# Optimization experiments

Measured on AMD Instinct MI355X. Metric: run time of the kernel, lower is better.

## Reference

```python
import jax, jax.numpy as jnp
import numpy as np

B, T, NUM_SKILLS, CONCEPT_NUM, HIDDEN = 64, 200, 1024, 256, 1024


def setup_inputs() -> dict:
    key = jax.random.key(0)
    ks = jax.random.split(key, 12)
    s_in = 1.0 / np.sqrt(NUM_SKILLS)
    s_h = 1.0 / np.sqrt(HIDDEN)
    s_c = 1.0 / np.sqrt(CONCEPT_NUM)
    return {
        "q_hot": jax.random.normal(ks[0], (B, T, NUM_SKILLS), jnp.float32),
        "result": jax.random.randint(ks[1], (B, T), 0, 2, jnp.int32),
        "next_q_hot": jax.random.normal(ks[2], (B, T, NUM_SKILLS), jnp.float32),
        "concept_num": CONCEPT_NUM,
        # kc: Linear(num_skills -> concept_num)
        "W_kc": jax.random.uniform(ks[3], (CONCEPT_NUM, NUM_SKILLS), jnp.float32, -s_in, s_in),
        "b_kc": jax.random.uniform(ks[4], (CONCEPT_NUM,), jnp.float32, -s_in, s_in),
        # LSTM (input = 2*concept_num, hidden = HIDDEN), torch gate order i,f,g,o
        "W_ih": jax.random.uniform(ks[5], (4 * HIDDEN, 2 * CONCEPT_NUM), jnp.float32, -s_h, s_h),
        "W_hh": jax.random.uniform(ks[6], (4 * HIDDEN, HIDDEN), jnp.float32, -s_h, s_h),
        "b_ih": jax.random.uniform(ks[7], (4 * HIDDEN,), jnp.float32, -s_h, s_h),
        "b_hh": jax.random.uniform(ks[8], (4 * HIDDEN,), jnp.float32, -s_h, s_h),
        # state: Linear(hidden -> concept_num)
        "W_state": jax.random.uniform(ks[9], (CONCEPT_NUM, HIDDEN), jnp.float32, -s_h, s_h),
        "b_state": jax.random.uniform(ks[10], (CONCEPT_NUM,), jnp.float32, -s_h, s_h),
        # out: Linear(concept_num -> 1)
        "W_out": jax.random.uniform(ks[11], (1, CONCEPT_NUM), jnp.float32, -s_c, s_c),
        "b_out": jax.random.uniform(jax.random.fold_in(key, 99), (1,), jnp.float32, -s_c, s_c),
    }


def _lstm(x, W_ih, W_hh, b_ih, b_hh):
    # x: [B, T, In] batch_first; returns h_seq [B, T, H]
    H = W_hh.shape[1]
    xT = jnp.swapaxes(x, 0, 1)                      # [T, B, In]
    gx = jnp.einsum('tbi,gi->tbg', xT, W_ih) + b_ih + b_hh  # [T, B, 4H]
    h0 = jnp.zeros((x.shape[0], H), x.dtype)
    c0 = jnp.zeros((x.shape[0], H), x.dtype)

    def step(carry, g_t):
        h, c = carry
        g = g_t + h @ W_hh.T                        # [B, 4H]
        i, f, gg, o = jnp.split(g, 4, axis=-1)
        i, f, o = jax.nn.sigmoid(i), jax.nn.sigmoid(f), jax.nn.sigmoid(o)
        c = f * c + i * jnp.tanh(gg)
        h = o * jnp.tanh(c)
        return (h, c), h

    _, h_seq = jax.lax.scan(step, (h0, c0), gx)
    return jnp.swapaxes(h_seq, 0, 1)                # [B, T, H]


def reference(q_hot, result, next_q_hot, concept_num,
              W_kc, b_kc, W_ih, W_hh, b_ih, b_hh,
              W_state, b_state, W_out, b_out):
    kc_hot = q_hot @ W_kc.T + b_kc                  # [B, T, C]
    next_kc_hot = next_q_hot @ W_kc.T + b_kc        # [B, T, C]

    # Vectorized replacement of the python double loop:
    # result==1 -> [kc_hot, 0]; else -> [0, kc_hot]
    mask = (result == 1)[..., None].astype(kc_hot.dtype)  # [B, T, 1]
    kc_vec = jnp.concatenate([kc_hot * mask, kc_hot * (1.0 - mask)], axis=-1)  # [B,T,2C]

    h = _lstm(kc_vec, W_ih, W_hh, b_ih, b_hh)       # [B, T, H]
    stu_state = h @ W_state.T + b_state             # [B, T, C]
    knowledge_div = stu_state - next_kc_hot
    vector = knowledge_div * next_kc_hot
    res = vector @ W_out.T + b_out                  # [B, T, 1]
    return (res, stu_state)
```

## Files before the change

kernel.cpp:

```cpp
#include <hip/hip_runtime.h>
#include <math.h>


typedef unsigned short u16;
typedef unsigned long long u64;
typedef __bf16 bf16x8 __attribute__((ext_vector_type(8)));
typedef float floatx4 __attribute__((ext_vector_type(4)));

__device__ __forceinline__ float bf2f(u16 h) {
  unsigned int u = ((unsigned int)h) << 16;
  float f;
  __builtin_memcpy(&f, &u, 4);
  return f;
}
__device__ __forceinline__ u16 f2bf(float f) {
  unsigned int u;
  __builtin_memcpy(&u, &f, 4);
  u += 0x7FFFu + ((u >> 16) & 1u);
  return (u16)(u >> 16);
}
__device__ __forceinline__ float sigm(float x) { return 1.0f / (1.0f + __expf(-x)); }

__global__ void cvt_kernel(const float* __restrict__ in, u16* __restrict__ out) {
  const int i = blockIdx.x * 256 + threadIdx.x;
  const float4 v = ((const float4*)in)[i];
  ushort4 o;
  o.x = f2bf(v.x);
  o.y = f2bf(v.y);
  o.z = f2bf(v.z);
  o.w = f2bf(v.w);
  ((ushort4*)out)[i] = o;
}

template <class Epi>
__global__ __launch_bounds__(256, 2) void gemm_bt(const u16* __restrict__ A,
                                                  const u16* __restrict__ B,
                                                  int M, int N, int K, Epi epi) {
  __shared__ u16 As[128 * 32];
  __shared__ u16 Bs[128 * 32];
  const int tid = threadIdx.x;
  const int w = tid >> 6, lane = tid & 63;
  const int wm = w & 1, wn = w >> 1;
  const int bm = blockIdx.x * 128, bn = blockIdx.y * 128;
  const int lrow = lane & 15, lk8 = (lane >> 4) * 8;
  const int srow = lane >> 2;
  const int skc = (lane & 3) * 8;

  floatx4 acc[4][4] = {};

  for (int k0 = 0; k0 < K; k0 += 32) {
#pragma unroll
    for (int r = 0; r < 2; ++r) {
      const int seg = w * 2 + r;
      const int row = seg * 16 + srow;
      __builtin_amdgcn_global_load_lds(
          (const __attribute__((address_space(1))) unsigned int*)(A + (size_t)(bm + row) * K + k0 + skc),
          (__attribute__((address_space(3))) unsigned int*)(As + seg * 512), 16, 0, 0);
      __builtin_amdgcn_global_load_lds(
          (const __attribute__((address_space(1))) unsigned int*)(B + (size_t)(bn + row) * K + k0 + skc),
          (__attribute__((address_space(3))) unsigned int*)(Bs + seg * 512), 16, 0, 0);
    }
    __syncthreads();

    bf16x8 af[4], bfr[4];
#pragma unroll
    for (int i = 0; i < 4; ++i) {
      af[i] = *(const bf16x8*)(As + (wm * 64 + i * 16 + lrow) * 32 + lk8);
      bfr[i] = *(const bf16x8*)(Bs + (wn * 64 + i * 16 + lrow) * 32 + lk8);
    }
#pragma unroll
    for (int i = 0; i < 4; ++i)
#pragma unroll
      for (int j = 0; j < 4; ++j)
        acc[i][j] = __builtin_amdgcn_mfma_f32_16x16x32_bf16(af[i], bfr[j], acc[i][j], 0, 0, 0);
    __syncthreads();
  }

  const int rbase = bm + wm * 64 + (lane >> 4) * 4;
  const int cbase = bn + wn * 64 + lrow;
#pragma unroll
  for (int i = 0; i < 4; ++i)
#pragma unroll
    for (int j = 0; j < 4; ++j)
#pragma unroll
      for (int r = 0; r < 4; ++r)
        epi(rbase + i * 16 + r, cbase + j * 16, acc[i][j][r]);
}

struct EpiKcVec {
  const float* bkc;
  const int* result;
  u16* kcv;
  __device__ void operator()(int row, int col, float v) const {
    v += bkc[col];
    const int off = (result[row] == 1) ? 0 : 256;
    const size_t base = (size_t)row * 512;
    kcv[base + off + col] = f2bf(v);
    kcv[base + (256 - off) + col] = 0;
  }
};
struct EpiNk {
  const float* bkc;
  float* nk;
  __device__ void operator()(int row, int col, float v) const {
    nk[(size_t)row * 256 + col] = v + bkc[col];
  }
};
struct EpiGx {
  const float* bih;
  const float* bhh;
  u16* gx;
  __device__ void operator()(int row, int col, float v) const {
    v += bih[col] + bhh[col];
    const int b = row / 200, t = row - b * 200;
    gx[(size_t)(t * 64 + b) * 4096 + col] = f2bf(v);
  }
};
struct EpiStu {
  const float* bst;
  float* out;
  __device__ void operator()(int row, int col, float v) const {
    v += bst[col];
    const int b = row & 63, t = row >> 6;
    out[(size_t)(b * 200 + t) * 256 + col] = v;
  }
};

__global__ void init_kernel(u16* hseq, unsigned* flags) {
  const int i = blockIdx.x * 256 + threadIdx.x;
  ((u64*)hseq)[i] = 0ULL;
  if (blockIdx.x == 0) flags[threadIdx.x] = 0u;
}

__global__ __launch_bounds__(256, 1) void lstm_scan(const u16* __restrict__ Whh,
                                                    const u16* __restrict__ gx,
                                                    u16* __restrict__ hseq,
                                                    unsigned* __restrict__ flags) {
  __shared__ __align__(16) u16 Ab[16 * 1032];
  __shared__ float gbuf[4 * 256];
  __shared__ __align__(16) u16 hbuf[256];
  const int tid = threadIdx.x;
  const int w = tid >> 6;
  const int lane = tid & 63;
  const int lrow = lane & 15;
  const int lk8 = (lane >> 4) * 8;
  const int gb = blockIdx.x >> 6;
  const int gn = blockIdx.x & 63;
  const int bb = gb * 16;
  const int j0 = gn * 16;

  bf16x8 bfrag[32];
  {
    const u16* wp = Whh + (size_t)(w * 1024 + j0 + lrow) * 1024 + lk8;
#pragma unroll
    for (int ks = 0; ks < 32; ++ks) bfrag[ks] = *(const bf16x8*)(wp + ks * 32);
  }

  float c_state = 0.0f;
  const int um = tid >> 4, un = tid & 15;

  const u16* gxb = gx + (size_t)(bb + (lane >> 4) * 4) * 4096 + w * 1024 + j0 + lrow;
  u16 gcur[4];
  {
    const u16* gp = gxb;
    gcur[0] = gp[0];
    gcur[1] = gp[4096];
    gcur[2] = gp[8192];
    gcur[3] = gp[12288];
  }

  for (int t = 0; t < 200; ++t) {
    {
      const u64* hs = (const u64*)(hseq + (size_t)t * 65536 + (size_t)bb * 1024);
      u64 tmp[16];
#pragma unroll
      for (int jj = 0; jj < 16; ++jj)
        tmp[jj] = __hip_atomic_load(hs + jj * 256 + tid, __ATOMIC_RELAXED,
                                    __HIP_MEMORY_SCOPE_AGENT);
#pragma unroll
      for (int jj = 0; jj < 16; ++jj) {
        const int ch = jj * 256 + tid;
        const int row = ch >> 8;
        const int cc = (ch & 255) * 4;
        *(u64*)(Ab + row * 1032 + cc) = tmp[jj];
      }
    }
    __syncthreads();

    floatx4 acc;
    acc[0] = bf2f(gcur[0]);
    acc[1] = bf2f(gcur[1]);
    acc[2] = bf2f(gcur[2]);
    acc[3] = bf2f(gcur[3]);
#pragma unroll
    for (int ks = 0; ks < 32; ++ks) {
      bf16x8 a = *(const bf16x8*)(Ab + lrow * 1032 + ks * 32 + lk8);
      acc = __builtin_amdgcn_mfma_f32_16x16x32_bf16(a, bfrag[ks], acc, 0, 0, 0);
    }
    {
      const int mrow = (lane >> 4) * 4;
#pragma unroll
      for (int r = 0; r < 4; ++r) gbuf[w * 256 + (mrow + r) * 16 + lrow] = acc[r];
    }
    __syncthreads();

    const float gi = gbuf[tid];
    const float gf = gbuf[256 + tid];
    const float gg = gbuf[512 + tid];
    const float go = gbuf[768 + tid];
    c_state = sigm(gf) * c_state + sigm(gi) * tanhf(gg);
    const float h = sigm(go) * tanhf(c_state);
    hbuf[um * 16 + un] = f2bf(h);
    __syncthreads();

    if (tid < 64) {
      const int row = lane >> 2, ck = lane & 3;
      const u64 v = *(const u64*)(hbuf + row * 16 + ck * 4);
      u64 old = __hip_atomic_exchange(
          (u64*)(hseq + (size_t)(t + 1) * 65536 + (size_t)(bb + row) * 1024 + j0 + ck * 4),
          v, __ATOMIC_RELAXED, __HIP_MEMORY_SCOPE_AGENT);
      asm volatile("" ::"v"(old));
      asm volatile("s_waitcnt vmcnt(0)" ::: "memory");
      if (lane == 0)
        __hip_atomic_store(&flags[blockIdx.x], (unsigned)(t + 1), __ATOMIC_RELAXED,
                           __HIP_MEMORY_SCOPE_AGENT);
    }

    if (t < 199) {
      const u16* gp = gxb + (size_t)(t + 1) * 64 * 4096;
      gcur[0] = gp[0];
      gcur[1] = gp[4096];
      gcur[2] = gp[8192];
      gcur[3] = gp[12288];
    }

    if (tid < 64) {
      const unsigned tgt = (unsigned)(t + 1);
      const unsigned* gf64 = &flags[gb * 64 + lane];
      for (;;) {
        const unsigned v = __hip_atomic_load(gf64, __ATOMIC_RELAXED,
                                             __HIP_MEMORY_SCOPE_AGENT);
        if (__all(v >= tgt)) break;
        __builtin_amdgcn_s_sleep(1);
      }
    }
    __syncthreads();
  }
}

__global__ void res_kernel(const float* __restrict__ stu, const float* __restrict__ nk,
                           const float* __restrict__ Wout, const float* __restrict__ bout,
                           float* __restrict__ res) {
  const int row = blockIdx.x * 4 + (threadIdx.x >> 6);
  const int lane = threadIdx.x & 63;
  const float* sp = stu + (size_t)row * 256;
  const float* np = nk + (size_t)row * 256;
  float s = 0.0f;
#pragma unroll
  for (int j = 0; j < 4; ++j) {
    const int c = j * 64 + lane;
    const float nv = np[c];
    s += (sp[c] - nv) * nv * Wout[c];
  }
#pragma unroll
  for (int o = 32; o > 0; o >>= 1) s += __shfl_down(s, o, 64);
  if (lane == 0) res[row] = s + bout[0];
}

extern "C" void kernel_launch(void* const* d_in, const int* in_sizes, int n_in,
                              void* d_out, int out_size, void* d_ws, size_t ws_size,
                              hipStream_t stream) {
  const float* q_hot = (const float*)d_in[0];
  const int* result = (const int*)d_in[1];
  const float* next_q = (const float*)d_in[2];
  const float* W_kc = (const float*)d_in[4];
  const float* b_kc = (const float*)d_in[5];
  const float* W_ih = (const float*)d_in[6];
  const float* W_hh = (const float*)d_in[7];
  const float* b_ih = (const float*)d_in[8];
  const float* b_hh = (const float*)d_in[9];
  const float* W_state = (const float*)d_in[10];
  const float* b_state = (const float*)d_in[11];
  const float* W_out = (const float*)d_in[12];
  const float* b_out = (const float*)d_in[13];

  float* out_res = (float*)d_out;
  float* out_stu = out_res + 12800;

  char* ws = (char*)d_ws;
  u16* kcv = (u16*)(ws);
  float* nk = (float*)(ws + 13107200);
  u16* hseq = (u16*)(ws + 26214400);
  u16* Whh_bf = (u16*)(ws + 52559872);
  u16* Wih_bf = (u16*)(ws + 60948480);
  u16* Wkc_bf = (u16*)(ws + 65142784);
  u16* Wst_bf = (u16*)(ws + 65667072);
  unsigned* flags = (unsigned*)(ws + 66191360);
  u16* gx = (u16*)(ws + 66192384);
  u16* q_bf = gx;
  u16* nq_bf = gx + 13107200;

  cvt_kernel<<<dim3(12800), 256, 0, stream>>>(q_hot, q_bf);
  cvt_kernel<<<dim3(12800), 256, 0, stream>>>(next_q, nq_bf);
  cvt_kernel<<<dim3(256), 256, 0, stream>>>(W_kc, Wkc_bf);
  cvt_kernel<<<dim3(2048), 256, 0, stream>>>(W_ih, Wih_bf);
  cvt_kernel<<<dim3(4096), 256, 0, stream>>>(W_hh, Whh_bf);
  cvt_kernel<<<dim3(256), 256, 0, stream>>>(W_state, Wst_bf);

  init_kernel<<<dim3(64), 256, 0, stream>>>(hseq, flags);
  gemm_bt<EpiKcVec><<<dim3(100, 2), 256, 0, stream>>>(q_bf, Wkc_bf, 12800, 256, 1024,
                                                      EpiKcVec{b_kc, result, kcv});
  gemm_bt<EpiNk><<<dim3(100, 2), 256, 0, stream>>>(nq_bf, Wkc_bf, 12800, 256, 1024,
                                                   EpiNk{b_kc, nk});
  gemm_bt<EpiGx><<<dim3(100, 32), 256, 0, stream>>>(kcv, Wih_bf, 12800, 4096, 512,
                                                    EpiGx{b_ih, b_hh, gx});
  lstm_scan<<<dim3(256), 256, 0, stream>>>(Whh_bf, gx, hseq, flags);
  gemm_bt<EpiStu><<<dim3(100, 2), 256, 0, stream>>>(hseq + 65536, Wst_bf, 12800, 256, 1024,
                                                    EpiStu{b_state, out_stu});
  res_kernel<<<dim3(3200), 256, 0, stream>>>(out_stu, nk, W_out, b_out, out_res);
}
```

Before: 1.342 ms.

## Replace flag-based LSTM step sync with tagged hidden-state words in a ring buffer

The scan no longer publishes h and then sets a per-block flag that the other blocks poll. Each 64-bit word now carries two bf16 hidden values plus the step index as a tag. Consumers spin on those tagged words in a 4-slot ring buffer, which removes the flag round trip and two block barriers per step. The MFMA chain is also split into four independent accumulators for more instruction-level parallelism, and the next step's gx values are prefetched earlier. In exchange, every step reads twice as many words and polls on data instead of flags. Correctness now depends on bounded skew between blocks, since the ring has only 4 slots, and on reusing the kcv workspace for the ring.

```diff
diff --git a/kernel.cpp b/kernel.cpp
--- a/kernel.cpp
+++ b/kernel.cpp
@@ -126,19 +126,16 @@
   }
 };
 
-__global__ void init_kernel(u16* hseq, unsigned* flags) {
-  const int i = blockIdx.x * 256 + threadIdx.x;
-  ((u64*)hseq)[i] = 0ULL;
-  if (blockIdx.x == 0) flags[threadIdx.x] = 0u;
+__global__ void init_kernel(u64* __restrict__ htag) {
+  htag[blockIdx.x * 256 + threadIdx.x] = 0ULL;
 }
 
 __global__ __launch_bounds__(256, 1) void lstm_scan(const u16* __restrict__ Whh,
                                                     const u16* __restrict__ gx,
                                                     u16* __restrict__ hseq,
-                                                    unsigned* __restrict__ flags) {
+                                                    u64* __restrict__ htag) {
   __shared__ __align__(16) u16 Ab[16 * 1032];
   __shared__ float gbuf[4 * 256];
-  __shared__ __align__(16) u16 hbuf[256];
   const int tid = threadIdx.x;
   const int w = tid >> 6;
   const int lane = tid & 63;
@@ -158,6 +155,7 @@
 
   float c_state = 0.0f;
   const int um = tid >> 4, un = tid & 15;
+  const int pub = !(tid & 1);
 
   const u16* gxb = gx + (size_t)(bb + (lane >> 4) * 4) * 4096 + w * 1024 + j0 + lrow;
   u16 gcur[4];
@@ -171,32 +169,58 @@
 
   for (int t = 0; t < 200; ++t) {
     {
-      const u64* hs = (const u64*)(hseq + (size_t)t * 65536 + (size_t)bb * 1024);
-      u64 tmp[16];
-#pragma unroll
-      for (int jj = 0; jj < 16; ++jj)
-        tmp[jj] = __hip_atomic_load(hs + jj * 256 + tid, __ATOMIC_RELAXED,
+      const unsigned want = (unsigned)t;
+      const u64* hw = htag + (size_t)(t & 3) * 32768 + (size_t)bb * 512 + tid;
+      u64 tmp[32];
+#pragma unroll
+      for (int jj = 0; jj < 32; ++jj)
+        tmp[jj] = __hip_atomic_load(hw + jj * 256, __ATOMIC_RELAXED,
                                     __HIP_MEMORY_SCOPE_AGENT);
-#pragma unroll
-      for (int jj = 0; jj < 16; ++jj) {
+      for (;;) {
+        bool ok = true;
+#pragma unroll
+        for (int jj = 0; jj < 32; ++jj) ok &= ((unsigned)(tmp[jj] >> 32) == want);
+        if (ok) break;
+        __builtin_amdgcn_s_sleep(1);
+#pragma unroll
+        for (int jj = 0; jj < 32; ++jj)
+          if ((unsigned)(tmp[jj] >> 32) != want)
+            tmp[jj] = __hip_atomic_load(hw + jj * 256, __ATOMIC_RELAXED,
+                                        __HIP_MEMORY_SCOPE_AGENT);
+      }
+#pragma unroll
+      for (int jj = 0; jj < 32; ++jj) {
         const int ch = jj * 256 + tid;
-        const int row = ch >> 8;
-        const int cc = (ch & 255) * 4;
-        *(u64*)(Ab + row * 1032 + cc) = tmp[jj];
+        const int row = ch >> 9;
+        const int cp = ch & 511;
+        *(unsigned*)(Ab + row * 1032 + cp * 2) = (unsigned)tmp[jj];
       }
     }
     __syncthreads();
 
-    floatx4 acc;
-    acc[0] = bf2f(gcur[0]);
-    acc[1] = bf2f(gcur[1]);
-    acc[2] = bf2f(gcur[2]);
-    acc[3] = bf2f(gcur[3]);
-#pragma unroll
-    for (int ks = 0; ks < 32; ++ks) {
-      bf16x8 a = *(const bf16x8*)(Ab + lrow * 1032 + ks * 32 + lk8);
-      acc = __builtin_amdgcn_mfma_f32_16x16x32_bf16(a, bfrag[ks], acc, 0, 0, 0);
-    }
+    floatx4 a0, a1 = {}, a2 = {}, a3 = {};
+    a0[0] = bf2f(gcur[0]);
+    a0[1] = bf2f(gcur[1]);
+    a0[2] = bf2f(gcur[2]);
+    a0[3] = bf2f(gcur[3]);
+
+    if (t < 199) {
+      const u16* gp = gxb + (size_t)(t + 1) * 262144;
+      gcur[0] = gp[0];
+      gcur[1] = gp[4096];
+      gcur[2] = gp[8192];
+      gcur[3] = gp[12288];
+    }
+
+#pragma unroll
+    for (int ks = 0; ks < 32; ks += 4) {
+      const u16* ap = Ab + lrow * 1032 + ks * 32 + lk8;
+      a0 = __builtin_amdgcn_mfma_f32_16x16x32_bf16(*(const bf16x8*)(ap), bfrag[ks], a0, 0, 0, 0);
+      a1 = __builtin_amdgcn_mfma_f32_16x16x32_bf16(*(const bf16x8*)(ap + 32), bfrag[ks + 1], a1, 0, 0, 0);
+      a2 = __builtin_amdgcn_mfma_f32_16x16x32_bf16(*(const bf16x8*)(ap + 64), bfrag[ks + 2], a2, 0, 0, 0);
+      a3 = __builtin_amdgcn_mfma_f32_16x16x32_bf16(*(const bf16x8*)(ap + 96), bfrag[ks + 3], a3, 0, 0, 0);
+    }
+    const floatx4 acc = (a0 + a1) + (a2 + a3);
     {
       const int mrow = (lane >> 4) * 4;
 #pragma unroll
@@ -210,41 +234,20 @@
     const float go = gbuf[768 + tid];
     c_state = sigm(gf) * c_state + sigm(gi) * tanhf(gg);
     const float h = sigm(go) * tanhf(c_state);
-    hbuf[um * 16 + un] = f2bf(h);
-    __syncthreads();
-
-    if (tid < 64) {
-      const int row = lane >> 2, ck = lane & 3;
-      const u64 v = *(const u64*)(hbuf + row * 16 + ck * 4);
-      u64 old = __hip_atomic_exchange(
-          (u64*)(hseq + (size_t)(t + 1) * 65536 + (size_t)(bb + row) * 1024 + j0 + ck * 4),
-          v, __ATOMIC_RELAXED, __HIP_MEMORY_SCOPE_AGENT);
-      asm volatile("" ::"v"(old));
-      asm volatile("s_waitcnt vmcnt(0)" ::: "memory");
-      if (lane == 0)
-        __hip_atomic_store(&flags[blockIdx.x], (unsigned)(t + 1), __ATOMIC_RELAXED,
-                           __HIP_MEMORY_SCOPE_AGENT);
-    }
-
-    if (t < 199) {
-      const u16* gp = gxb + (size_t)(t + 1) * 64 * 4096;
-      gcur[0] = gp[0];
-      gcur[1] = gp[4096];
-      gcur[2] = gp[8192];
-      gcur[3] = gp[12288];
-    }
-
-    if (tid < 64) {
-      const unsigned tgt = (unsigned)(t + 1);
-      const unsigned* gf64 = &flags[gb * 64 + lane];
-      for (;;) {
-        const unsigned v = __hip_atomic_load(gf64, __ATOMIC_RELAXED,
-                                             __HIP_MEMORY_SCOPE_AGENT);
-        if (__all(v >= tgt)) break;
-        __builtin_amdgcn_s_sleep(1);
+
+    {
+      const unsigned hb = (unsigned)f2bf(h);
+      const unsigned ob = (unsigned)__shfl_xor((int)hb, 1, 64);
+      if (pub) {
+        const unsigned lo = hb | (ob << 16);
+        const u64 word = ((u64)(unsigned)(t + 1) << 32) | (u64)lo;
+        __hip_atomic_store(htag + (size_t)((t + 1) & 3) * 32768 +
+                               (size_t)(bb + um) * 512 + gn * 8 + (un >> 1),
+                           word, __ATOMIC_RELAXED, __HIP_MEMORY_SCOPE_AGENT);
+        *(unsigned*)(hseq + (size_t)(t + 1) * 65536 + (size_t)(bb + um) * 1024 +
+                     j0 + un) = lo;
       }
     }
-    __syncthreads();
   }
 }
 
@@ -289,13 +292,13 @@
 
   char* ws = (char*)d_ws;
   u16* kcv = (u16*)(ws);
+  u64* htag = (u64*)(ws);
   float* nk = (float*)(ws + 13107200);
   u16* hseq = (u16*)(ws + 26214400);
   u16* Whh_bf = (u16*)(ws + 52559872);
   u16* Wih_bf = (u16*)(ws + 60948480);
   u16* Wkc_bf = (u16*)(ws + 65142784);
   u16* Wst_bf = (u16*)(ws + 65667072);
-  unsigned* flags = (unsigned*)(ws + 66191360);
   u16* gx = (u16*)(ws + 66192384);
   u16* q_bf = gx;
   u16* nq_bf = gx + 13107200;
@@ -307,14 +310,14 @@
   cvt_kernel<<<dim3(4096), 256, 0, stream>>>(W_hh, Whh_bf);
   cvt_kernel<<<dim3(256), 256, 0, stream>>>(W_state, Wst_bf);
 
-  init_kernel<<<dim3(64), 256, 0, stream>>>(hseq, flags);
   gemm_bt<EpiKcVec><<<dim3(100, 2), 256, 0, stream>>>(q_bf, Wkc_bf, 12800, 256, 1024,
                                                       EpiKcVec{b_kc, result, kcv});
   gemm_bt<EpiNk><<<dim3(100, 2), 256, 0, stream>>>(nq_bf, Wkc_bf, 12800, 256, 1024,
                                                    EpiNk{b_kc, nk});
   gemm_bt<EpiGx><<<dim3(100, 32), 256, 0, stream>>>(kcv, Wih_bf, 12800, 4096, 512,
                                                     EpiGx{b_ih, b_hh, gx});
-  lstm_scan<<<dim3(256), 256, 0, stream>>>(Whh_bf, gx, hseq, flags);
+  init_kernel<<<dim3(512), 256, 0, stream>>>(htag);
+  lstm_scan<<<dim3(256), 256, 0, stream>>>(Whh_bf, gx, hseq, htag);
   gemm_bt<EpiStu><<<dim3(100, 2), 256, 0, stream>>>(hseq + 65536, Wst_bf, 12800, 256, 1024,
                                                     EpiStu{b_state, out_stu});
   res_kernel<<<dim3(3200), 256, 0, stream>>>(out_stu, nk, W_out, b_out, out_res);
```

Measured after the change: 1.399 ms. 1.04x slower.

## Halve LSTM scan blocks with 512-thread workgroups and split MFMA accumulators

Applied to the files above, without the earlier changes.

Restructures the persistent LSTM scan from 256 blocks of 256 threads to 128 blocks of 512 threads. Each block now owns 32 hidden columns, which halves both the number of participants in each per-batch-group flag barrier and the redundant reloads of h per block. It also loads h with 16-byte cache-bypassing inline-asm loads, prefetches the next gx before the MFMA chain, and splits the MFMA chain into four independent accumulators to shorten the dependency latency. Per-block work per step doubles and the launch bounds change, which may raise register pressure since each thread still holds 32 weight fragments.

```diff
diff --git a/kernel.cpp b/kernel.cpp
--- a/kernel.cpp
+++ b/kernel.cpp
@@ -6,6 +6,7 @@
 typedef unsigned long long u64;
 typedef __bf16 bf16x8 __attribute__((ext_vector_type(8)));
 typedef float floatx4 __attribute__((ext_vector_type(4)));
+typedef unsigned int u32x4 __attribute__((ext_vector_type(4)));
 
 __device__ __forceinline__ float bf2f(u16 h) {
   unsigned int u = ((unsigned int)h) << 16;
@@ -129,37 +130,40 @@
 __global__ void init_kernel(u16* hseq, unsigned* flags) {
   const int i = blockIdx.x * 256 + threadIdx.x;
   ((u64*)hseq)[i] = 0ULL;
-  if (blockIdx.x == 0) flags[threadIdx.x] = 0u;
-}
-
-__global__ __launch_bounds__(256, 1) void lstm_scan(const u16* __restrict__ Whh,
+  if (blockIdx.x == 0 && threadIdx.x < 128) flags[threadIdx.x] = 0u;
+}
+
+__global__ __launch_bounds__(512, 2) void lstm_scan(const u16* __restrict__ Whh,
                                                     const u16* __restrict__ gx,
                                                     u16* __restrict__ hseq,
                                                     unsigned* __restrict__ flags) {
   __shared__ __align__(16) u16 Ab[16 * 1032];
-  __shared__ float gbuf[4 * 256];
-  __shared__ __align__(16) u16 hbuf[256];
+  __shared__ float gbuf[4 * 512];
+  __shared__ __align__(16) u16 hbuf[16 * 32];
   const int tid = threadIdx.x;
   const int w = tid >> 6;
   const int lane = tid & 63;
   const int lrow = lane & 15;
   const int lk8 = (lane >> 4) * 8;
-  const int gb = blockIdx.x >> 6;
-  const int gn = blockIdx.x & 63;
+  const int g = w & 3;
+  const int hf = w >> 2;
+  const int gb = blockIdx.x >> 5;
+  const int gn = blockIdx.x & 31;
   const int bb = gb * 16;
-  const int j0 = gn * 16;
+  const int j0 = gn * 32;
 
   bf16x8 bfrag[32];
   {
-    const u16* wp = Whh + (size_t)(w * 1024 + j0 + lrow) * 1024 + lk8;
+    const u16* wp = Whh + (size_t)(g * 1024 + j0 + hf * 16 + lrow) * 1024 + lk8;
 #pragma unroll
     for (int ks = 0; ks < 32; ++ks) bfrag[ks] = *(const bf16x8*)(wp + ks * 32);
   }
 
   float c_state = 0.0f;
-  const int um = tid >> 4, un = tid & 15;
-
-  const u16* gxb = gx + (size_t)(bb + (lane >> 4) * 4) * 4096 + w * 1024 + j0 + lrow;
+  const int um = tid >> 5, un = tid & 31;
+
+  const u16* gxb =
+      gx + (size_t)(bb + (lane >> 4) * 4) * 4096 + g * 1024 + j0 + hf * 16 + lrow;
   u16 gcur[4];
   {
     const u16* gp = gxb;
@@ -171,74 +175,101 @@
 
   for (int t = 0; t < 200; ++t) {
     {
-      const u64* hs = (const u64*)(hseq + (size_t)t * 65536 + (size_t)bb * 1024);
-      u64 tmp[16];
-#pragma unroll
-      for (int jj = 0; jj < 16; ++jj)
-        tmp[jj] = __hip_atomic_load(hs + jj * 256 + tid, __ATOMIC_RELAXED,
-                                    __HIP_MEMORY_SCOPE_AGENT);
-#pragma unroll
-      for (int jj = 0; jj < 16; ++jj) {
-        const int ch = jj * 256 + tid;
-        const int row = ch >> 8;
-        const int cc = (ch & 255) * 4;
-        *(u64*)(Ab + row * 1032 + cc) = tmp[jj];
-      }
-    }
-    __syncthreads();
-
-    floatx4 acc;
-    acc[0] = bf2f(gcur[0]);
-    acc[1] = bf2f(gcur[1]);
-    acc[2] = bf2f(gcur[2]);
-    acc[3] = bf2f(gcur[3]);
-#pragma unroll
-    for (int ks = 0; ks < 32; ++ks) {
-      bf16x8 a = *(const bf16x8*)(Ab + lrow * 1032 + ks * 32 + lk8);
-      acc = __builtin_amdgcn_mfma_f32_16x16x32_bf16(a, bfrag[ks], acc, 0, 0, 0);
-    }
+      const char* hb = (const char*)(hseq + (size_t)t * 65536 + (size_t)bb * 1024);
+      const char* p0 = hb + tid * 16;
+      const char* p1 = p0 + 8192;
+      const char* p2 = p0 + 16384;
+      const char* p3 = p0 + 24576;
+      u32x4 t0, t1, t2, t3;
+      asm volatile(
+          "global_load_dwordx4 %0, %4, off sc0 sc1\n\t"
+          "global_load_dwordx4 %1, %5, off sc0 sc1\n\t"
+          "global_load_dwordx4 %2, %6, off sc0 sc1\n\t"
+          "global_load_dwordx4 %3, %7, off sc0 sc1\n\t"
+          "s_waitcnt vmcnt(0)"
+          : "=&v"(t0), "=&v"(t1), "=&v"(t2), "=&v"(t3)
+          : "v"(p0), "v"(p1), "v"(p2), "v"(p3)
+          : "memory");
+      {
+        const int ch = tid;
+        *(u32x4*)(Ab + (ch >> 7) * 1032 + (ch & 127) * 8) = t0;
+      }
+      {
+        const int ch = 512 + tid;
+        *(u32x4*)(Ab + (ch >> 7) * 1032 + (ch & 127) * 8) = t1;
+      }
+      {
+        const int ch = 1024 + tid;
+        *(u32x4*)(Ab + (ch >> 7) * 1032 + (ch & 127) * 8) = t2;
+      }
+      {
+        const int ch = 1536 + tid;
+        *(u32x4*)(Ab + (ch >> 7) * 1032 + (ch & 127) * 8) = t3;
+      }
+    }
+    __syncthreads();
+
+    floatx4 a0, a1 = {}, a2 = {}, a3 = {};
+    a0[0] = bf2f(gcur[0]);
+    a0[1] = bf2f(gcur[1]);
+    a0[2] = bf2f(gcur[2]);
+    a0[3] = bf2f(gcur[3]);
+
+    if (t < 199) {
+      const u16* gp = gxb + (size_t)(t + 1) * 262144;
+      gcur[0] = gp[0];
+      gcur[1] = gp[4096];
+      gcur[2] = gp[8192];
+      gcur[3] = gp[12288];
+    }
+
+#pragma unroll
+    for (int ks = 0; ks < 32; ks += 4) {
+      const u16* ap = Ab + lrow * 1032 + ks * 32 + lk8;
+      a0 = __builtin_amdgcn_mfma_f32_16x16x32_bf16(*(const bf16x8*)(ap), bfrag[ks], a0, 0, 0, 0);
+      a1 = __builtin_amdgcn_mfma_f32_16x16x32_bf16(*(const bf16x8*)(ap + 32), bfrag[ks + 1], a1, 0, 0, 0);
+      a2 = __builtin_amdgcn_mfma_f32_16x16x32_bf16(*(const bf16x8*)(ap + 64), bfrag[ks + 2], a2, 0, 0, 0);
+      a3 = __builtin_amdgcn_mfma_f32_16x16x32_bf16(*(const bf16x8*)(ap + 96), bfrag[ks + 3], a3, 0, 0, 0);
+    }
+    const floatx4 acc = (a0 + a1) + (a2 + a3);
     {
       const int mrow = (lane >> 4) * 4;
 #pragma unroll
-      for (int r = 0; r < 4; ++r) gbuf[w * 256 + (mrow + r) * 16 + lrow] = acc[r];
-    }
-    __syncthreads();
-
-    const float gi = gbuf[tid];
-    const float gf = gbuf[256 + tid];
-    const float gg = gbuf[512 + tid];
-    const float go = gbuf[768 + tid];
+      for (int r = 0; r < 4; ++r)
+        gbuf[g * 512 + (mrow + r) * 32 + hf * 16 + lrow] = acc[r];
+    }
+    __syncthreads();
+
+    const float gi = gbuf[um * 32 + un];
+    const float gf = gbuf[512 + um * 32 + un];
+    const float gg = gbuf[1024 + um * 32 + un];
+    const float go = gbuf[1536 + um * 32 + un];
     c_state = sigm(gf) * c_state + sigm(gi) * tanhf(gg);
     const float h = sigm(go) * tanhf(c_state);
-    hbuf[um * 16 + un] = f2bf(h);
+    hbuf[um * 32 + un] = f2bf(h);
     __syncthreads();
 
     if (tid < 64) {
-      const int row = lane >> 2, ck = lane & 3;
-      const u64 v = *(const u64*)(hbuf + row * 16 + ck * 4);
-      u64 old = __hip_atomic_exchange(
-          (u64*)(hseq + (size_t)(t + 1) * 65536 + (size_t)(bb + row) * 1024 + j0 + ck * 4),
-          v, __ATOMIC_RELAXED, __HIP_MEMORY_SCOPE_AGENT);
-      asm volatile("" ::"v"(old));
+#pragma unroll
+      for (int k = 0; k < 2; ++k) {
+        const int wi = k * 64 + lane;
+        const int row = wi >> 3, cw = wi & 7;
+        const u64 v = *(const u64*)(hbuf + row * 32 + cw * 4);
+        u64 old = __hip_atomic_exchange(
+            (u64*)(hseq + (size_t)(t + 1) * 65536 + (size_t)(bb + row) * 1024 +
+                   j0 + cw * 4),
+            v, __ATOMIC_RELAXED, __HIP_MEMORY_SCOPE_AGENT);
+        asm volatile("" ::"v"(old));
+      }
       asm volatile("s_waitcnt vmcnt(0)" ::: "memory");
       if (lane == 0)
         __hip_atomic_store(&flags[blockIdx.x], (unsigned)(t + 1), __ATOMIC_RELAXED,
                            __HIP_MEMORY_SCOPE_AGENT);
-    }
-
-    if (t < 199) {
-      const u16* gp = gxb + (size_t)(t + 1) * 64 * 4096;
-      gcur[0] = gp[0];
-      gcur[1] = gp[4096];
-      gcur[2] = gp[8192];
-      gcur[3] = gp[12288];
-    }
-
-    if (tid < 64) {
+
       const unsigned tgt = (unsigned)(t + 1);
-      const unsigned* gf64 = &flags[gb * 64 + lane];
+      const unsigned* gfp = &flags[gb * 32 + (lane & 31)];
       for (;;) {
-        const unsigned v = __hip_atomic_load(gf64, __ATOMIC_RELAXED,
+        const unsigned v = __hip_atomic_load(gfp, __ATOMIC_RELAXED,
                                              __HIP_MEMORY_SCOPE_AGENT);
         if (__all(v >= tgt)) break;
         __builtin_amdgcn_s_sleep(1);
@@ -314,7 +345,7 @@
                                                    EpiNk{b_kc, nk});
   gemm_bt<EpiGx><<<dim3(100, 32), 256, 0, stream>>>(kcv, Wih_bf, 12800, 4096, 512,
                                                     EpiGx{b_ih, b_hh, gx});
-  lstm_scan<<<dim3(256), 256, 0, stream>>>(Whh_bf, gx, hseq, flags);
+  lstm_scan<<<dim3(128), 512, 0, stream>>>(Whh_bf, gx, hseq, flags);
   gemm_bt<EpiStu><<<dim3(100, 2), 256, 0, stream>>>(hseq + 65536, Wst_bf, 12800, 256, 1024,
                                                     EpiStu{b_state, out_stu});
   res_kernel<<<dim3(3200), 256, 0, stream>>>(out_stu, nk, W_out, b_out, out_res);
```

After: 1.268 ms. 1.06x faster.
